# Kernel optimization log

Hardware: AMD Instinct MI355X
Metric: run time of the kernel (lower is better)

The kernel has to match this reference:

```python
import jax, jax.numpy as jnp
import numpy as np

BASE = 10000.0

def rotate_half(x):
    # interleaved pairs: (x0, x1, x2, x3, ...) -> (-x1, x0, -x3, x2, ...)
    x2 = x.reshape(x.shape[:-1] + (-1, 2))
    a, b = x2[..., 0], x2[..., 1]
    return jnp.stack((-b, a), axis=-1).reshape(x.shape)

def rope_tables(seq_len, head_dim, dtype):
    inv_freq = 1.0 / (BASE ** (jnp.arange(0, head_dim, 2, dtype=jnp.float32) / head_dim))
    t = jnp.arange(seq_len, dtype=jnp.float32)
    freqs = jnp.outer(t, inv_freq)                      # [s, head_dim//2]
    cos = jnp.repeat(jnp.cos(freqs), 2, axis=-1)        # '... d -> ... (d 2)'
    sin = jnp.repeat(jnp.sin(freqs), 2, axis=-1)
    # seq_dimension = -3 for [b, s, h, d] tensors -> broadcast over heads
    return cos[:, None, :].astype(dtype), sin[:, None, :].astype(dtype)

def setup_inputs() -> dict:
    key = jax.random.key(0)
    kx, kw1, kw2 = jax.random.split(key, 3)
    b, s, d = 4, 2048, 2048
    h = 16
    x = jax.random.normal(kx, (b, s, d), dtype=jnp.float32)
    # causal mask: True above the diagonal = masked positions
    attn_mask = jnp.triu(jnp.ones((s, s), dtype=bool), k=1)
    Wqkv_w = jax.random.normal(kw1, (d, 3 * d), dtype=jnp.float32) / np.sqrt(d)
    Wqkv_b = jnp.zeros((3 * d,), dtype=jnp.float32)
    Wout_w = jax.random.normal(kw2, (d, d), dtype=jnp.float32) / np.sqrt(d)
    Wout_b = jnp.zeros((d,), dtype=jnp.float32)
    return {"x": x, "attn_mask": attn_mask, "Wqkv_w": Wqkv_w, "Wqkv_b": Wqkv_b,
            "Wout_w": Wout_w, "Wout_b": Wout_b, "num_heads": 16}

def reference(x, attn_mask, Wqkv_w, Wqkv_b, Wout_w, Wout_b, num_heads):
    b, s, d = x.shape
    h = num_heads
    hd = d // h
    qkv = jnp.einsum('bsd,de->bse', x, Wqkv_w) + Wqkv_b        # [b, s, 3d]
    qkv = qkv.reshape(b, s, 3, h, hd)
    q, k, v = qkv[:, :, 0], qkv[:, :, 1], qkv[:, :, 2]          # [b, s, h, hd]
    cos, sin = rope_tables(s, hd, x.dtype)                      # [s, 1, hd]
    q = q * cos + rotate_half(q) * sin
    k = k * cos + rotate_half(k) * sin
    scale = 1.0 / np.sqrt(hd).astype(np.float32)
    scores = jnp.einsum('bqhd,bkhd->bhqk', q, k) * scale        # [b, h, s, s]
    scores = jnp.where(attn_mask, -jnp.inf, scores)
    attn = jax.nn.softmax(scores, axis=-1)
    ctx = jnp.einsum('bhqk,bkhd->bqhd', attn, v)                # [b, s, h, hd]
    ctx = ctx.reshape(b, s, d)
    return jnp.einsum('bsd,de->bse', ctx, Wout_w) + Wout_b
```

## Files before the change

### kernel.cpp

```cpp
#include <hip/hip_runtime.h>

#define BB 4
#define SS 2048
#define DD 2048
#define HH 16
#define HD 128
#define D3 6144

typedef __attribute__((ext_vector_type(8))) short short8;
typedef __attribute__((ext_vector_type(4))) float float4v;

#define MFMA16(a, b, c) __builtin_amdgcn_mfma_f32_16x16x32_bf16(a, b, c, 0, 0, 0)

#define GLL16(g, l)                                                     \
    __builtin_amdgcn_global_load_lds(                                   \
        (__attribute__((address_space(1))) void*)(g),                   \
        (__attribute__((address_space(3))) void*)(l), 16, 0, 0)

__device__ __forceinline__ unsigned short f2b(float f) {
    union { float f; unsigned u; } v;
    v.f = f;
    unsigned r = v.u + 0x7FFFu + ((v.u >> 16) & 1u);
    return (unsigned short)(r >> 16);
}
__device__ __forceinline__ float b2f(unsigned short h) {
    union { unsigned u; float f; } v;
    v.u = ((unsigned)h) << 16;
    return v.f;
}

__global__ void cast_f32_bf16(const float* __restrict__ in,
                              unsigned short* __restrict__ out) {
    int i = (blockIdx.x * 256 + threadIdx.x) * 4;
    float4 v = *(const float4*)(in + i);
    ushort4 o;
    o.x = f2b(v.x); o.y = f2b(v.y); o.z = f2b(v.z); o.w = f2b(v.w);
    *(ushort4*)(out + i) = o;
}

__global__ void transpose_cast(const float* __restrict__ in,
                               unsigned short* __restrict__ out, int R, int C) {
    __shared__ float tile[32][33];
    int c0 = blockIdx.x * 32, r0 = blockIdx.y * 32;
    int tc = threadIdx.x & 31, tr = threadIdx.x >> 5;
#pragma unroll
    for (int i = 0; i < 4; ++i) {
        int r = tr + i * 8;
        tile[r][tc] = in[(size_t)(r0 + r) * C + c0 + tc];
    }
    __syncthreads();
#pragma unroll
    for (int i = 0; i < 4; ++i) {
        int wr = tr + i * 8;
        out[(size_t)(c0 + wr) * R + r0 + tc] = f2b(tile[tc][wr]);
    }
}

__global__ void vtrans(const unsigned short* __restrict__ qkv,
                       unsigned short* __restrict__ vT) {
    __shared__ unsigned short tile[32][33];
    int bh = blockIdx.z, b = bh >> 4, h = bh & 15;
    int s0 = blockIdx.x * 32, d0 = blockIdx.y * 32;
    int tc = threadIdx.x & 31, tr = threadIdx.x >> 5;
    const unsigned short* src = qkv + (size_t)b * SS * D3 + 4096 + h * HD;
#pragma unroll
    for (int i = 0; i < 4; ++i) {
        int sl = tr + i * 8;
        tile[sl][tc] = src[(size_t)(s0 + sl) * D3 + d0 + tc];
    }
    __syncthreads();
    unsigned short* dst = vT + (size_t)bh * HD * SS;
#pragma unroll
    for (int i = 0; i < 4; ++i) {
        int dl = tr + i * 8;
        dst[(size_t)(d0 + dl) * SS + s0 + tc] = tile[tc][dl];
    }
}

template <int BF16OUT>
__global__ __launch_bounds__(512, 2) void gemm256(
    const unsigned short* __restrict__ A,
    const unsigned short* __restrict__ Bt,
    const float* __restrict__ bias,
    void* __restrict__ Cout, int M, int N, int K) {
    __shared__ unsigned short As[4][256 * 32];
    __shared__ unsigned short Bs[4][256 * 32];

    const int n0 = blockIdx.x * 256, m0 = blockIdx.y * 256;
    const int t = threadIdx.x, lane = t & 63, w = t >> 6;
    const int quad = lane >> 4, lr = lane & 15;
    const int wm = (w >> 2) * 128, wn = (w & 3) * 64;

    const int sr = lane >> 2;
    const int sc = ((lane & 3) ^ ((lane >> 3) & 3)) * 8;
    const unsigned short* Ag = A + (size_t)(m0 + w * 16 + sr) * K + sc;
    const unsigned short* Bg = Bt + (size_t)(n0 + w * 16 + sr) * K + sc;

    const int rsw = (quad ^ ((lr >> 1) & 3)) * 8;

    float4v acc[8][4] = {};
    short8 af0[4], af1[4], b0[2], b1[2];

#define SA(buf, rb, k0) \
    GLL16(Ag + (size_t)(rb) * K + (k0), &As[buf][((rb) + w * 16) * 32])
#define SB(buf, rb, k0) \
    GLL16(Bg + (size_t)(rb) * K + (k0), &Bs[buf][((rb) + w * 16) * 32])
#define STAGE_A(buf, k0) do { SA(buf, 0, k0); SA(buf, 128, k0); } while (0)
#define STAGE_B(buf, k0) do { SB(buf, 0, k0); SB(buf, 128, k0); } while (0)
#define LDA(dst, mh)                                                         \
    do {                                                                     \
        _Pragma("unroll") for (int i = 0; i < 4; ++i)                        \
            dst[i] = *(const short8*)&As[cur][                               \
                (wm + (mh)*64 + i * 16 + lr) * 32 + rsw];                    \
    } while (0)
#define LDB(dst, nh)                                                         \
    do {                                                                     \
        _Pragma("unroll") for (int j = 0; j < 2; ++j)                        \
            dst[j] = *(const short8*)&Bs[cur][                               \
                (wn + (nh)*32 + j * 16 + lr) * 32 + rsw];                    \
    } while (0)
#define MMQ(ar, br, io, jo)                                                  \
    do {                                                                     \
        _Pragma("unroll") for (int i = 0; i < 4; ++i)                        \
            _Pragma("unroll") for (int j = 0; j < 2; ++j)                    \
                acc[(io) + i][(jo) + j] = MFMA16(                            \
                    ar[i], br[j], acc[(io) + i][(jo) + j]);                  \
    } while (0)
#define MM2(ar, br0, io, jo0, br1, jo1)                                      \
    do {                                                                     \
        __builtin_amdgcn_s_setprio(1);                                       \
        MMQ(ar, br0, io, jo0);                                               \
        MMQ(ar, br1, io, jo1);                                               \
        __builtin_amdgcn_s_setprio(0);                                       \
    } while (0)
#define WAIT_LGKM0()                                                         \
    do {                                                                     \
        asm volatile("s_waitcnt lgkmcnt(0)" ::: "memory");                   \
        __builtin_amdgcn_sched_barrier(0);                                   \
    } while (0)

    const int NT = K >> 5;
    STAGE_A(0, 0);  STAGE_B(0, 0);
    STAGE_A(1, 32); STAGE_B(1, 32);
    STAGE_A(2, 64); STAGE_B(2, 64);
    asm volatile("s_waitcnt vmcnt(8)" ::: "memory");
    __builtin_amdgcn_s_barrier();

    for (int tk = 0; tk < NT; ++tk) {
        const int cur = tk & 3;
        const int b3 = (tk + 3) & 3;
        int t3 = tk + 3; if (t3 >= NT) t3 -= NT;
        const int k3 = t3 << 5;

        LDA(af0, 0);
        LDB(b0, 0);
        LDB(b1, 1);
        STAGE_A(b3, k3);
        __builtin_amdgcn_s_barrier();
        WAIT_LGKM0();
        MM2(af0, b0, 0, 0, b1, 2);
        __builtin_amdgcn_s_barrier();
        LDA(af1, 1);
        STAGE_B(b3, k3);
        __builtin_amdgcn_s_barrier();
        WAIT_LGKM0();
        MM2(af1, b1, 4, 2, b0, 0);
        asm volatile("s_waitcnt vmcnt(8)" ::: "memory");
        __builtin_amdgcn_s_barrier();
    }
    asm volatile("s_waitcnt vmcnt(0)" ::: "memory");

#pragma unroll
    for (int jj = 0; jj < 4; ++jj) {
        const int n = n0 + wn + jj * 16 + lr;
        const float bv = bias[n];
#pragma unroll
        for (int ii = 0; ii < 8; ++ii)
#pragma unroll
            for (int r = 0; r < 4; ++r) {
                const int m = m0 + wm + ii * 16 + quad * 4 + r;
                const float v = acc[ii][jj][r] + bv;
                if (BF16OUT)
                    ((unsigned short*)Cout)[(size_t)m * N + n] = f2b(v);
                else
                    ((float*)Cout)[(size_t)m * N + n] = v;
            }
    }
#undef SA
#undef SB
#undef STAGE_A
#undef STAGE_B
#undef LDA
#undef LDB
#undef MMQ
#undef MM2
#undef WAIT_LGKM0
}

__global__ void rope_kernel(unsigned short* __restrict__ qkv) {
    int tid = blockIdx.x * 256 + threadIdx.x;
    int i4 = tid & 15;
    int h = (tid >> 4) & 15;
    int s = (tid >> 8) & 2047;
    int b = tid >> 19;
    size_t off = ((size_t)(b * SS + s)) * D3 + h * HD + i4 * 8;
    unsigned short* q = qkv + off;
    unsigned short* k = q + 2048;
    short8 qv = *(short8*)q, kv = *(short8*)k;
    const float L2IF = 0.2076205059304601f;
    const float R2PI = 0.15915494309189535f;
    short8 qo, ko;
#pragma unroll
    for (int j = 0; j < 4; ++j) {
        int i = i4 * 4 + j;
        float invr = exp2f(-(float)i * L2IF) * R2PI;
        float rev = (float)s * invr;
        float rr = rev - floorf(rev);
        float sn = __builtin_amdgcn_sinf(rr);
        float cs = __builtin_amdgcn_cosf(rr);
        float a0 = b2f((unsigned short)qv[2 * j]);
        float a1 = b2f((unsigned short)qv[2 * j + 1]);
        qo[2 * j] = (short)f2b(a0 * cs - a1 * sn);
        qo[2 * j + 1] = (short)f2b(a1 * cs + a0 * sn);
        float c0 = b2f((unsigned short)kv[2 * j]);
        float c1 = b2f((unsigned short)kv[2 * j + 1]);
        ko[2 * j] = (short)f2b(c0 * cs - c1 * sn);
        ko[2 * j + 1] = (short)f2b(c1 * cs + c0 * sn);
    }
    *(short8*)q = qo;
    *(short8*)k = ko;
}

__global__ __launch_bounds__(256) void attn_kernel(
    const unsigned short* __restrict__ qkv,
    const unsigned short* __restrict__ vT,
    unsigned short* __restrict__ ctx) {
    __shared__ unsigned short Ks[2][64 * 128];
    __shared__ unsigned short Vs[2][128 * 64];
    __shared__ unsigned short PT[4][32][40];
    const int bh = blockIdx.y, b = bh >> 4, h = bh & 15;
    const int t = threadIdx.x, w = t >> 6, lane = t & 63;
    const int quad = lane >> 4, lr = lane & 15;
    const unsigned short* qbase = qkv + (size_t)b * SS * D3 + h * HD;
    const unsigned short* kbase = qbase + 2048;
    const unsigned short* vtb = vT + (size_t)bh * HD * SS;
    const float SCL2E = 0.12751741769976451f;
    const float NB16 = -23.083120654223414f;
    const int q0a = blockIdx.x * 128;
    const int q0b = (15 - (int)blockIdx.x) * 128;
    const int nta = (q0a >> 6) + 2, ntb = (q0b >> 6) + 2, ntot = nta + ntb;
    const int kr = lane >> 4, kg = lane & 15;
    const int vr = lane >> 3, vg = lane & 7;

    auto stage = [&](int k0, int bi) {
        unsigned short* KD = Ks[bi];
        unsigned short* VD = Vs[bi];
#pragma unroll
        for (int u = 0; u < 4; ++u) {
            int row = w * 16 + u * 4 + kr;
            int g = kg ^ (row & 15);
            GLL16(kbase + (size_t)(k0 + row) * D3 + g * 8,
                  &KD[(w * 16 + u * 4) * 128]);
        }
#pragma unroll
        for (int u = 0; u < 4; ++u) {
            int row = w * 32 + u * 8 + vr;
            int g = vg ^ (row & 7);
            GLL16(vtb + (size_t)row * SS + k0 + g * 8,
                  &VD[(w * 32 + u * 8) * 64]);
        }
    };

    int wq = q0a + w * 32;
    short8 qf[2][4];
#pragma unroll
    for (int m = 0; m < 2; ++m)
#pragma unroll
        for (int c = 0; c < 4; ++c)
            qf[m][c] = *(const short8*)(qbase + (size_t)(wq + m * 16 + lr) * D3 +
                                        c * 32 + quad * 8);

    float4v o[2][8] = {};
    float l_lane[2] = {0.f, 0.f};

    auto epilogue = [&]() {
#pragma unroll
        for (int m = 0; m < 2; ++m) {
            float l = l_lane[m];
            l += __shfl_xor(l, 16);
            l += __shfl_xor(l, 32);
#pragma unroll
            for (int r = 0; r < 4; ++r) {
                float linv = 1.0f / __shfl(l, quad * 4 + r);
#pragma unroll
                for (int dc = 0; dc < 8; ++dc) {
                    float val = o[m][dc][r] * linv;
                    ctx[(size_t)(b * SS + wq + m * 16 + quad * 4 + r) * DD +
                        h * HD + dc * 16 + lr] = f2b(val);
                }
            }
        }
    };

    stage(0, 0);

    for (int it = 0; it < ntot; ++it) {
        __syncthreads();
        int nit = it + 1;
        if (nit < ntot) stage((nit < nta ? nit : nit - nta) * 64, nit & 1);
        int k0 = (it < nta ? it : it - nta) * 64;
        const unsigned short* KB = Ks[it & 1];
        const unsigned short* VB = Vs[it & 1];

        if (k0 <= wq + 31) {
            float4v sc[2][4] = {};
#pragma unroll
            for (int c = 0; c < 4; ++c) {
                short8 kf[4];
#pragma unroll
                for (int ks = 0; ks < 4; ++ks)
                    kf[ks] = *(const short8*)&KB[(ks * 16 + lr) * 128 +
                                                 (((c * 4 + quad) ^ lr) * 8)];
#pragma unroll
                for (int ks = 0; ks < 4; ++ks) {
                    sc[0][ks] = MFMA16(kf[ks], qf[0][c], sc[0][ks]);
                    sc[1][ks] = MFMA16(kf[ks], qf[1][c], sc[1][ks]);
                }
            }
            const bool nm = (k0 + 63 > wq);
#pragma unroll
            for (int kc = 0; kc < 2; ++kc) {
#pragma unroll
                for (int m = 0; m < 2; ++m)
#pragma unroll
                    for (int ks2 = 0; ks2 < 2; ++ks2) {
                        int ks = kc * 2 + ks2;
                        unsigned pk[2];
#pragma unroll
                        for (int rp = 0; rp < 2; ++rp) {
                            unsigned lo = 0, hi = 0;
#pragma unroll
                            for (int rr = 0; rr < 2; ++rr) {
                                int r = rp * 2 + rr;
                                float p = exp2f(fmaf(sc[m][ks][r], SCL2E, NB16));
                                if (nm) {
                                    int key = k0 + ks * 16 + quad * 4 + r;
                                    if (key > wq + m * 16 + lr) p = 0.0f;
                                }
                                l_lane[m] += p;
                                union { float f; unsigned u; } pu;
                                pu.f = p;
                                if (rr == 0) lo = pu.u >> 16;
                                else hi = pu.u >> 16;
                            }
                            pk[rp] = lo | (hi << 16);
                        }
                        uint2 pkk = {pk[0], pk[1]};
                        *(uint2*)&PT[w][m * 16 + lr][ks2 * 16 + quad * 4] = pkk;
                    }
                short8 pf0 = *(const short8*)&PT[w][lr][quad * 8];
                short8 pf1 = *(const short8*)&PT[w][16 + lr][quad * 8];
#pragma unroll
                for (int dc = 0; dc < 8; ++dc) {
                    short8 vf = *(const short8*)&VB[(dc * 16 + lr) * 64 +
                                                    (((kc * 4 + quad) ^ (lr & 7)) * 8)];
                    o[0][dc] = MFMA16(pf0, vf, o[0][dc]);
                    o[1][dc] = MFMA16(pf1, vf, o[1][dc]);
                }
            }
        }

        if (it == nta - 1) {
            epilogue();
#pragma unroll
            for (int m = 0; m < 2; ++m) {
                l_lane[m] = 0.f;
#pragma unroll
                for (int dc = 0; dc < 8; ++dc) o[m][dc] = (float4v){0, 0, 0, 0};
            }
            wq = q0b + w * 32;
#pragma unroll
            for (int m = 0; m < 2; ++m)
#pragma unroll
                for (int c = 0; c < 4; ++c)
                    qf[m][c] = *(const short8*)(qbase +
                                                (size_t)(wq + m * 16 + lr) * D3 +
                                                c * 32 + quad * 8);
        }
    }
    epilogue();
}

extern "C" void kernel_launch(void* const* d_in, const int* in_sizes, int n_in,
                              void* d_out, int out_size, void* d_ws, size_t ws_size,
                              hipStream_t stream) {
    const float* x = (const float*)d_in[0];
    const float* Wqkv_w = (const float*)d_in[2];
    const float* Wqkv_b = (const float*)d_in[3];
    const float* Wout_w = (const float*)d_in[4];
    const float* Wout_b = (const float*)d_in[5];
    float* out = (float*)d_out;

    unsigned short* x_bf = (unsigned short*)d_ws;
    unsigned short* wqkv_t = x_bf + 16777216;
    unsigned short* wout_t = wqkv_t + 12582912;
    unsigned short* qkv = wout_t + 4194304;
    unsigned short* ctx = qkv + 50331648;
    unsigned short* vT = x_bf;

    cast_f32_bf16<<<16384, 256, 0, stream>>>(x, x_bf);
    transpose_cast<<<dim3(192, 64), 256, 0, stream>>>(Wqkv_w, wqkv_t, 2048, 6144);
    transpose_cast<<<dim3(64, 64), 256, 0, stream>>>(Wout_w, wout_t, 2048, 2048);
    gemm256<1><<<dim3(24, 32), 512, 0, stream>>>(x_bf, wqkv_t, Wqkv_b, qkv,
                                                 8192, 6144, 2048);
    rope_kernel<<<8192, 256, 0, stream>>>(qkv);
    vtrans<<<dim3(64, 4, 64), 256, 0, stream>>>(qkv, vT);
    attn_kernel<<<dim3(8, 64), 256, 0, stream>>>(qkv, vT, ctx);
    gemm256<0><<<dim3(8, 32), 512, 0, stream>>>(ctx, wout_t, Wout_b, out,
                                                8192, 2048, 2048);
}
```

Measured before the change: 686.0 us.

## Software-pipeline LDS fragment loads across k-tiles in GEMM main loop

Restructures the GEMM main loop to unroll by two k-tiles with even/odd register sets, prefetching the next tile's A/B fragments from LDS while MFMAs of the current half-tile run, using partial lgkmcnt waits instead of full drains. This aims to hide LDS read latency behind matrix math. It increases register usage (extra fragment buffers), which may reduce occupancy or cause spills, and the vmcnt waits were tightened.

```diff
diff --git a/kernel.cpp b/kernel.cpp
--- a/kernel.cpp
+++ b/kernel.cpp
@@ -99,7 +99,7 @@
     const int rsw = (quad ^ ((lr >> 1) & 3)) * 8;
 
     float4v acc[8][4] = {};
-    short8 af0[4], af1[4], b0[2], b1[2];
+    short8 af0E[4], af0O[4], af1[4], b0E[2], b0O[2], b1E[2], b1O[2];
 
 #define SA(buf, rb, k0) \
     GLL16(Ag + (size_t)(rb) * K + (k0), &As[buf][((rb) + w * 16) * 32])
@@ -107,16 +107,16 @@
     GLL16(Bg + (size_t)(rb) * K + (k0), &Bs[buf][((rb) + w * 16) * 32])
 #define STAGE_A(buf, k0) do { SA(buf, 0, k0); SA(buf, 128, k0); } while (0)
 #define STAGE_B(buf, k0) do { SB(buf, 0, k0); SB(buf, 128, k0); } while (0)
-#define LDA(dst, mh)                                                         \
+#define LDA(dst, BASE, mh)                                                   \
     do {                                                                     \
         _Pragma("unroll") for (int i = 0; i < 4; ++i)                        \
-            dst[i] = *(const short8*)&As[cur][                               \
+            dst[i] = *(const short8*)&(BASE)[                                \
                 (wm + (mh)*64 + i * 16 + lr) * 32 + rsw];                    \
     } while (0)
-#define LDB(dst, nh)                                                         \
+#define LDB(dst, BASE, nh)                                                   \
     do {                                                                     \
         _Pragma("unroll") for (int j = 0; j < 2; ++j)                        \
-            dst[j] = *(const short8*)&Bs[cur][                               \
+            dst[j] = *(const short8*)&(BASE)[                                \
                 (wn + (nh)*32 + j * 16 + lr) * 32 + rsw];                    \
     } while (0)
 #define MMQ(ar, br, io, jo)                                                  \
@@ -133,9 +133,9 @@
         MMQ(ar, br1, io, jo1);                                               \
         __builtin_amdgcn_s_setprio(0);                                       \
     } while (0)
-#define WAIT_LGKM0()                                                         \
+#define LGKM(n)                                                              \
     do {                                                                     \
-        asm volatile("s_waitcnt lgkmcnt(0)" ::: "memory");                   \
+        asm volatile("s_waitcnt lgkmcnt(" #n ")" ::: "memory");              \
         __builtin_amdgcn_sched_barrier(0);                                   \
     } while (0)
 
@@ -145,27 +145,45 @@
     STAGE_A(2, 64); STAGE_B(2, 64);
     asm volatile("s_waitcnt vmcnt(8)" ::: "memory");
     __builtin_amdgcn_s_barrier();
-
-    for (int tk = 0; tk < NT; ++tk) {
-        const int cur = tk & 3;
-        const int b3 = (tk + 3) & 3;
-        int t3 = tk + 3; if (t3 >= NT) t3 -= NT;
-        const int k3 = t3 << 5;
-
-        LDA(af0, 0);
-        LDB(b0, 0);
-        LDB(b1, 1);
-        STAGE_A(b3, k3);
-        __builtin_amdgcn_s_barrier();
-        WAIT_LGKM0();
-        MM2(af0, b0, 0, 0, b1, 2);
-        __builtin_amdgcn_s_barrier();
-        LDA(af1, 1);
-        STAGE_B(b3, k3);
-        __builtin_amdgcn_s_barrier();
-        WAIT_LGKM0();
-        MM2(af1, b1, 4, 2, b0, 0);
-        asm volatile("s_waitcnt vmcnt(8)" ::: "memory");
+    LDA(af0E, As[0], 0); LDB(b0E, Bs[0], 0); LDB(b1E, Bs[0], 1);
+
+    for (int u = 0; u < (NT >> 1); ++u) {
+        const int te = 2 * u, to = 2 * u + 1;
+        const unsigned short* ASe = As[te & 3];
+        const unsigned short* ASo = As[to & 3];
+        const unsigned short* BSo = Bs[to & 3];
+        const unsigned short* ASn = As[(te + 2) & 3];
+        const unsigned short* BSn = Bs[(te + 2) & 3];
+        const int b3e = (te + 3) & 3, b3o = (to + 3) & 3;
+        int t3e = te + 3; if (t3e >= NT) t3e -= NT;
+        int t3o = to + 3; if (t3o >= NT) t3o -= NT;
+        const int k3e = t3e << 5, k3o = t3o << 5;
+
+        STAGE_A(b3e, k3e);
+        LDA(af1, ASe, 1);
+        __builtin_amdgcn_s_barrier();
+        LGKM(4);
+        MM2(af0E, b0E, 0, 0, b1E, 2);
+        asm volatile("s_waitcnt vmcnt(6)" ::: "memory");
+        __builtin_amdgcn_s_barrier();
+        STAGE_B(b3e, k3e);
+        LDA(af0O, ASo, 0); LDB(b0O, BSo, 0); LDB(b1O, BSo, 1);
+        __builtin_amdgcn_s_barrier();
+        LGKM(8);
+        MM2(af1, b1E, 4, 2, b0E, 0);
+        __builtin_amdgcn_s_barrier();
+        STAGE_A(b3o, k3o);
+        LDA(af1, ASo, 1);
+        __builtin_amdgcn_s_barrier();
+        LGKM(4);
+        MM2(af0O, b0O, 0, 0, b1O, 2);
+        asm volatile("s_waitcnt vmcnt(6)" ::: "memory");
+        __builtin_amdgcn_s_barrier();
+        STAGE_B(b3o, k3o);
+        LDA(af0E, ASn, 0); LDB(b0E, BSn, 0); LDB(b1E, BSn, 1);
+        __builtin_amdgcn_s_barrier();
+        LGKM(8);
+        MM2(af1, b1O, 4, 2, b0O, 0);
         __builtin_amdgcn_s_barrier();
     }
     asm volatile("s_waitcnt vmcnt(0)" ::: "memory");
@@ -194,7 +212,7 @@
 #undef LDB
 #undef MMQ
 #undef MM2
-#undef WAIT_LGKM0
+#undef LGKM
 }
 
 __global__ void rope_kernel(unsigned short* __restrict__ qkv) {
```

Result: slower. 787.4 us (+14.8%).
